# Performance work log

Hardware: AMD Instinct MI355X
Metric: run time of the kernel (lower is better)

Reference implementation:

```python
import jax, jax.numpy as jnp
import numpy as np

NUM_HEADS = 16
BN_EPS = 1e-3  # tf.layers.BatchNormalization default epsilon


def _z_norm(a, axis, scale):
    mu = jnp.mean(a, axis=axis, keepdims=True)
    sd = jnp.std(a, axis=axis, keepdims=True)
    return (a - mu) / (sd * scale + 1e-10)


def setup_inputs() -> dict:
    key = jax.random.key(0)
    ks = jax.random.split(key, 12)
    B, S, D = 4, 1024, 1024
    w = lambda k: jax.random.normal(k, (D, D), dtype=jnp.float32) * 0.02
    return {
        'q': jax.random.normal(ks[0], (B, S, D), dtype=jnp.float32),
        'k': jax.random.normal(ks[1], (B, S, D), dtype=jnp.float32),
        'v': jax.random.normal(ks[2], (B, S, D), dtype=jnp.float32),
        'mask': jax.random.randint(ks[3], (B, 1, S, S), 0, 2, dtype=jnp.int32),
        'is_training': 0,
        'q_gamma': jnp.ones((D,), jnp.float32),
        'q_beta': jnp.zeros((D,), jnp.float32),
        'q_mean': jax.random.normal(ks[4], (D,), dtype=jnp.float32) * 0.1,
        'q_var': jnp.ones((D,), jnp.float32),
        'Wq': w(ks[5]), 'bq': jnp.zeros((D,), jnp.float32),
        'Wqq': w(ks[6]), 'bqq': jnp.zeros((D,), jnp.float32),
        'Wo': w(ks[7]), 'bo': jnp.zeros((D,), jnp.float32),
    }


def reference(q, k, v, mask, is_training, q_gamma, q_beta, q_mean, q_var,
              Wq, bq, Wqq, bqq, Wo, bo):
    B, S, D = q.shape
    H = NUM_HEADS
    dh = D // H
    # BatchNorm (inference mode: call() passes no training flag -> moving stats)
    x = (q - q_mean) * jax.lax.rsqrt(q_var + BN_EPS) * q_gamma + q_beta
    # q = wqq(relu(wq(.)))  (k/v projections are dead: call() sets k = v = q)
    x = jax.nn.relu(x @ Wq + bq)
    x = x @ Wqq + bqq
    qh = x.reshape(B, S, H, dh).transpose(0, 2, 1, 3)  # [B,H,S,dh]
    logits = jnp.einsum('bhqd,bhkd->bhqk', qh, qh) / jnp.sqrt(jnp.float32(dh))
    logits = logits + mask.astype(logits.dtype) * -1e9
    attn = jax.nn.softmax(logits, axis=3)  # [B,H,S,S]
    last = jnp.mean(logits, axis=-1, keepdims=True)        # [B,H,S,1]
    last2 = jnp.mean(logits, axis=(2, 3), keepdims=True)   # [B,H,1,1]
    w_within = jax.nn.softmax(_z_norm(last, 2, 2), axis=2)   # softmax over queries
    w_betw = jax.nn.softmax(_z_norm(last2, 1, 2), axis=1)    # softmax over heads
    attn = attn * w_within * w_betw
    out = jnp.einsum('bhqk,bhkd->bhqd', attn, qh)           # v == qh
    out = out.transpose(0, 2, 1, 3).reshape(B, S, D)
    out = out @ Wo + bo
    return out, attn
```

## Files before the change

### kernel.cpp

```cpp
#include <hip/hip_runtime.h>
#include <math.h>


constexpr int Bz = 4, S = 1024, D = 1024, H = 16, DH = 64;
constexpr int N_ROWS = Bz * S;
#define BN_EPS 1e-3f
#define NEG_BIG -1e9f

typedef __attribute__((ext_vector_type(8))) short bf16x8;
typedef __attribute__((ext_vector_type(8))) unsigned short u16x8;
typedef __attribute__((ext_vector_type(4))) unsigned short u16x4;
typedef __attribute__((ext_vector_type(4))) float f32x4;

__device__ inline unsigned short f2bf(float f) {
  union { float f; unsigned int u; } v; v.f = f;
  unsigned int u = v.u;
  return (unsigned short)((u + 0x7FFFu + ((u >> 16) & 1u)) >> 16);
}
__device__ inline float bf2f(unsigned short h) {
  union { unsigned int u; float f; } v; v.u = ((unsigned int)h) << 16;
  return v.f;
}

__global__ __launch_bounds__(256)
void k_prep_all(const float* __restrict__ W0, const float* __restrict__ W1,
                const float* __restrict__ W2, unsigned short* __restrict__ T0,
                unsigned short* __restrict__ T1, unsigned short* __restrict__ T2,
                const float* __restrict__ q, const float* __restrict__ gamma,
                const float* __restrict__ beta, const float* __restrict__ mean,
                const float* __restrict__ var, unsigned short* __restrict__ qbn,
                const int* __restrict__ mask, float* __restrict__ n_cnt2,
                float* __restrict__ cs) {
  __shared__ float Ls[64][65];
  const int bid = blockIdx.x, t = threadIdx.x;
  if (bid < 768) {
    const int z = bid >> 8, rem = bid & 255;
    const float* W = z == 0 ? W0 : (z == 1 ? W1 : W2);
    unsigned short* T = z == 0 ? T0 : (z == 1 ? T1 : T2);
    const int k0 = (rem & 15) * 64, n0 = (rem >> 4) * 64;
    {
      const int r = t >> 2, c0 = (t & 3) * 16;
#pragma unroll
      for (int i = 0; i < 4; ++i) {
        float4 f = *(const float4*)&W[(size_t)(k0 + r) * 1024 + n0 + c0 + 4 * i];
        Ls[r][c0 + 4 * i] = f.x; Ls[r][c0 + 4 * i + 1] = f.y;
        Ls[r][c0 + 4 * i + 2] = f.z; Ls[r][c0 + 4 * i + 3] = f.w;
      }
    }
    __syncthreads();
    {
      const int d = t >> 2, c = t & 3;
      u16x8 o0, o1;
#pragma unroll
      for (int i = 0; i < 8; ++i) {
        o0[i] = f2bf(Ls[c * 16 + i][d]);
        o1[i] = f2bf(Ls[c * 16 + 8 + i][d]);
      }
      unsigned short* dst = &T[(size_t)(n0 + d) * 1024 + k0 + c * 16];
      *(u16x8*)dst = o0;
      *(u16x8*)(dst + 8) = o1;
    }
  } else if (bid < 2816) {
    const int id = bid - 768;
    const size_t e0 = ((size_t)id * 256 + t) * 8;
    const int col = (int)(e0 & 1023);
    float x[8], g[8], bb[8], mm[8], vv[8];
    *(float4*)&x[0] = *(const float4*)&q[e0];
    *(float4*)&x[4] = *(const float4*)&q[e0 + 4];
    *(float4*)&g[0] = *(const float4*)&gamma[col];
    *(float4*)&g[4] = *(const float4*)&gamma[col + 4];
    *(float4*)&bb[0] = *(const float4*)&beta[col];
    *(float4*)&bb[4] = *(const float4*)&beta[col + 4];
    *(float4*)&mm[0] = *(const float4*)&mean[col];
    *(float4*)&mm[4] = *(const float4*)&mean[col + 4];
    *(float4*)&vv[0] = *(const float4*)&var[col];
    *(float4*)&vv[4] = *(const float4*)&var[col + 4];
    bf16x8 o;
#pragma unroll
    for (int i = 0; i < 8; ++i) {
      float sc = g[i] * rsqrtf(vv[i] + BN_EPS);
      o[i] = (short)f2bf(fmaf(x[i], sc, bb[i] - mm[i] * sc));
    }
    *(bf16x8*)&qbn[e0] = o;
  } else if (bid < 2880) {
    const int id = bid - 2816;
    const int row = id * 64 + (t >> 2);
    const int4* mp = (const int4*)&mask[(size_t)row * 1024 + (t & 3) * 256];
    int s = 0;
#pragma unroll 8
    for (int i = 0; i < 64; ++i) { int4 m = mp[i]; s += (m.x + m.y) + (m.z + m.w); }
    s += __shfl_xor(s, 1, 64);
    s += __shfl_xor(s, 2, 64);
    if ((t & 3) == 0) n_cnt2[row] = (float)s;
  } else {
    const int id = bid - 2880;
    *(float4*)&cs[id * 1024 + t * 4] = make_float4(0.f, 0.f, 0.f, 0.f);
  }
}

template<bool RELU, bool OUTBF>
__global__ __launch_bounds__(256)
void k_gemm2(const unsigned short* __restrict__ A, const unsigned short* __restrict__ BT,
             const float* __restrict__ bias, void* __restrict__ C) {
  __shared__ unsigned short As[128 * 64];
  __shared__ unsigned short Bs[64 * 64];
  const int t = threadIdx.x;
  const int w = t >> 6, l = t & 63, l15 = l & 15, l4 = l >> 4;
  const int m0 = blockIdx.x * 128, n0 = blockIdx.y * 64;
  const int wm = (w >> 1) * 64, wn = (w & 1) * 32;

  f32x4 acc[4][2];
#pragma unroll
  for (int i = 0; i < 4; ++i)
#pragma unroll
    for (int j = 0; j < 2; ++j) acc[i][j] = (f32x4){0.f, 0.f, 0.f, 0.f};

  for (int k0 = 0; k0 < 1024; k0 += 64) {
    __syncthreads();
#pragma unroll
    for (int i = 0; i < 4; ++i) {
      const int c = i * 256 + t, row = c >> 3, slot = c & 7;
      bf16x8 v = *(const bf16x8*)&A[(size_t)(m0 + row) * 1024 + k0 + slot * 8];
      *(bf16x8*)((char*)As + row * 128 + ((slot * 16) ^ ((row & 7) << 4))) = v;
    }
#pragma unroll
    for (int i = 0; i < 2; ++i) {
      const int c = i * 256 + t, row = c >> 3, slot = c & 7;
      bf16x8 v = *(const bf16x8*)&BT[(size_t)(n0 + row) * 1024 + k0 + slot * 8];
      *(bf16x8*)((char*)Bs + row * 128 + ((slot * 16) ^ ((row & 7) << 4))) = v;
    }
    __syncthreads();
    bf16x8 af[4][2], bfr[2][2];
#pragma unroll
    for (int bm = 0; bm < 4; ++bm) {
      const int r = wm + bm * 16 + l15;
#pragma unroll
      for (int kk = 0; kk < 2; ++kk)
        af[bm][kk] = *(const bf16x8*)((const char*)As + r * 128 +
                                      ((kk * 64 + l4 * 16) ^ ((r & 7) << 4)));
    }
#pragma unroll
    for (int bn = 0; bn < 2; ++bn) {
      const int r = wn + bn * 16 + l15;
#pragma unroll
      for (int kk = 0; kk < 2; ++kk)
        bfr[bn][kk] = *(const bf16x8*)((const char*)Bs + r * 128 +
                                       ((kk * 64 + l4 * 16) ^ ((r & 7) << 4)));
    }
#pragma unroll
    for (int bm = 0; bm < 4; ++bm)
#pragma unroll
      for (int bn = 0; bn < 2; ++bn) {
        acc[bm][bn] = __builtin_amdgcn_mfma_f32_16x16x32_bf16(af[bm][0], bfr[bn][0], acc[bm][bn], 0, 0, 0);
        acc[bm][bn] = __builtin_amdgcn_mfma_f32_16x16x32_bf16(af[bm][1], bfr[bn][1], acc[bm][bn], 0, 0, 0);
      }
  }
  float bv[2];
#pragma unroll
  for (int bn = 0; bn < 2; ++bn) bv[bn] = bias[n0 + wn + bn * 16 + l15];
#pragma unroll
  for (int bm = 0; bm < 4; ++bm)
#pragma unroll
    for (int bn = 0; bn < 2; ++bn)
#pragma unroll
      for (int r = 0; r < 4; ++r) {
        float v = acc[bm][bn][r] + bv[bn];
        if (RELU) v = fmaxf(v, 0.f);
        const size_t idx = (size_t)(m0 + wm + bm * 16 + l4 * 4 + r) * 1024 +
                           n0 + wn + bn * 16 + l15;
        if (OUTBF) ((unsigned short*)C)[idx] = f2bf(v);
        else ((float*)C)[idx] = v;
      }
}

__global__ __launch_bounds__(256)
void k_cvt(const unsigned short* __restrict__ xqb, unsigned short* __restrict__ qhT,
           float* __restrict__ cs) {
  __shared__ unsigned short Ls[64][72];
  const int t = threadIdx.x;
  const int b = blockIdx.x >> 4;
  const int sb = (blockIdx.x & 15) * 64;
  const int h = blockIdx.y;
  {
    const int r = t >> 2, c0 = (t & 3) * 16;
    const unsigned short* src = &xqb[(size_t)(b * 1024 + sb + r) * 1024 + h * 64 + c0];
    u16x8 a = *(const u16x8*)src;
    u16x8 b8 = *(const u16x8*)(src + 8);
    *(u16x8*)&Ls[r][c0] = a;
    *(u16x8*)&Ls[r][c0 + 8] = b8;
  }
  __syncthreads();
  {
    const int d = t >> 2, c = t & 3;
    u16x8 o0, o1;
#pragma unroll
    for (int i = 0; i < 8; ++i) {
      o0[i] = Ls[c * 16 + i][d];
      o1[i] = Ls[c * 16 + 8 + i][d];
    }
    unsigned short* dst = &qhT[(size_t)((b * 16 + h) * 64 + d) * 1024 + sb + c * 16];
    *(u16x8*)dst = o0;
    *(u16x8*)(dst + 8) = o1;
  }
  if (t < 64) {
    float s = 0.f;
#pragma unroll 8
    for (int i = 0; i < 64; ++i) s += bf2f(Ls[i][t]);
    atomicAdd(&cs[b * 1024 + h * 64 + t], s);
  }
}

__global__ __launch_bounds__(256)
void k_suml2(const unsigned short* __restrict__ xqb, const float* __restrict__ cs,
             float* __restrict__ sum_l) {
  const int qc = blockIdx.x, b = blockIdx.y;
  const int t = threadIdx.x;
  const int h = t >> 4, dg = t & 15;
  const float4 c4 = *(const float4*)&cs[b * 1024 + t * 4];
  for (int qi = 0; qi < 64; ++qi) {
    const int q = qc * 64 + qi;
    u16x4 xv = *(const u16x4*)&xqb[(size_t)(b * 1024 + q) * 1024 + t * 4];
    float s = bf2f(xv[0]) * c4.x + bf2f(xv[1]) * c4.y +
              bf2f(xv[2]) * c4.z + bf2f(xv[3]) * c4.w;
    s += __shfl_xor(s, 1, 64);
    s += __shfl_xor(s, 2, 64);
    s += __shfl_xor(s, 4, 64);
    s += __shfl_xor(s, 8, 64);
    if (dg == 0) sum_l[(size_t)(b * 16 + h) * 1024 + q] = s * 0.125f;
  }
}

template<int PASS>
__global__ __launch_bounds__(256)
void k_attn5(const unsigned short* __restrict__ xqb, const int* __restrict__ mask,
             const unsigned short* __restrict__ qhT, const float* __restrict__ w_row,
             float* __restrict__ attn, unsigned short* __restrict__ pvb,
             float* __restrict__ denom) {
  __shared__ unsigned short Ks[2][64 * 64];
  __shared__ unsigned short Pst[PASS ? 4 * 16 * 64 : 8];

  const int t = threadIdx.x;
  const int w = t >> 6, l = t & 63;
  const int l15 = l & 15, l4 = l >> 4;
  const int q0 = blockIdx.x * 64;
  const int h = blockIdx.y, b = blockIdx.z;
  const int bh = b * 16 + h;

  bf16x8 qa0, qa1;
  {
    const unsigned short* qp =
        &xqb[(size_t)(b * 1024 + q0 + w * 16 + l15) * 1024 + h * 64 + l4 * 8];
    qa0 = *(const bf16x8*)qp;
    qa1 = *(const bf16x8*)(qp + 32);
  }

  float wsc[4];
  if (PASS == 1) {
#pragma unroll
    for (int r = 0; r < 4; ++r)
      wsc[r] = w_row[(size_t)bh * 1024 + q0 + w * 16 + l4 * 4 + r];
  }

  float dsum[4] = {0.f, 0.f, 0.f, 0.f};
  f32x4 vacc[4];
#pragma unroll
  for (int c = 0; c < 4; ++c) vacc[c] = (f32x4){0.f, 0.f, 0.f, 0.f};

  const int srow = t >> 3, sslot = t & 7;
  const int sswz = (sslot * 16) ^ ((srow & 7) << 4);
  const size_t sga = (size_t)(b * 1024 + srow) * 1024 + h * 64 + sslot * 8;

  bf16x8 s0 = *(const bf16x8*)&xqb[sga];
  bf16x8 s1 = *(const bf16x8*)&xqb[sga + 32 * 1024];
  *(bf16x8*)((char*)Ks[0] + srow * 128 + sswz) = s0;
  *(bf16x8*)((char*)Ks[0] + (srow + 32) * 128 + sswz) = s1;
  s0 = *(const bf16x8*)&xqb[sga + 64 * 1024];
  s1 = *(const bf16x8*)&xqb[sga + 96 * 1024];

  for (int ti = 0; ti < 16; ++ti) {
    __syncthreads();
    const int cur = ti & 1;
    if (ti < 15) {
      *(bf16x8*)((char*)Ks[cur ^ 1] + srow * 128 + sswz) = s0;
      *(bf16x8*)((char*)Ks[cur ^ 1] + (srow + 32) * 128 + sswz) = s1;
    }
    if (ti < 14) {
      s0 = *(const bf16x8*)&xqb[sga + (size_t)(ti + 2) * 65536];
      s1 = *(const bf16x8*)&xqb[sga + (size_t)(ti + 2) * 65536 + 32 * 1024];
    }
    const int k0 = ti * 64;

    f32x4 lacc[4];
#pragma unroll
    for (int c = 0; c < 4; ++c) {
      const int r = c * 16 + l15;
      const char* kb = (const char*)Ks[cur] + r * 128;
      const int rsw = (r & 7) << 4;
      bf16x8 kb0 = *(const bf16x8*)(kb + ((l4 * 16) ^ rsw));
      bf16x8 kb1 = *(const bf16x8*)(kb + ((64 + l4 * 16) ^ rsw));
      f32x4 z = (f32x4){0.f, 0.f, 0.f, 0.f};
      z = __builtin_amdgcn_mfma_f32_16x16x32_bf16(qa0, kb0, z, 0, 0, 0);
      z = __builtin_amdgcn_mfma_f32_16x16x32_bf16(qa1, kb1, z, 0, 0, 0);
      lacc[c] = z;
    }

    int mrr[4][4];
#pragma unroll
    for (int c = 0; c < 4; ++c)
#pragma unroll
      for (int r = 0; r < 4; ++r)
        mrr[c][r] = mask[(size_t)(b * 1024 + q0 + w * 16 + l4 * 4 + r) * 1024 +
                         k0 + c * 16 + l15];

#pragma unroll
    for (int c = 0; c < 4; ++c) {
#pragma unroll
      for (int r = 0; r < 4; ++r) {
        float p = __expf(fmaf((float)mrr[c][r], NEG_BIG, lacc[c][r] * 0.125f));
        if (PASS == 0) {
          dsum[r] += p;
        } else {
          attn[(size_t)(bh * 1024 + q0 + w * 16 + l4 * 4 + r) * 1024 +
               k0 + c * 16 + l15] = p * wsc[r];
          const int qq = l4 * 4 + r;
          *(unsigned short*)((char*)&Pst[w * 1024] + qq * 128 +
                             (((c * 16 + l15) * 2) ^ ((qq & 7) << 4))) = f2bf(p);
        }
      }
    }

    if (PASS == 1) {
#pragma unroll
      for (int kk = 0; kk < 2; ++kk) {
        const char* pb = (const char*)&Pst[w * 1024] + l15 * 128;
        bf16x8 pa = *(const bf16x8*)(pb + ((kk * 64 + l4 * 16) ^ ((l15 & 7) << 4)));
#pragma unroll
        for (int c = 0; c < 4; ++c) {
          bf16x8 vb = *(const bf16x8*)&qhT[(size_t)(bh * 64 + c * 16 + l15) * 1024 +
                                           k0 + kk * 32 + l4 * 8];
          vacc[c] = __builtin_amdgcn_mfma_f32_16x16x32_bf16(pa, vb, vacc[c], 0, 0, 0);
        }
      }
    }
  }

  if (PASS == 0) {
#pragma unroll
    for (int r = 0; r < 4; ++r) {
      float d2 = dsum[r];
#pragma unroll
      for (int m = 1; m < 16; m <<= 1) d2 += __shfl_xor(d2, m, 64);
      if (l15 == 0)
        denom[(size_t)bh * 1024 + q0 + w * 16 + l4 * 4 + r] = d2;
    }
  } else {
#pragma unroll
    for (int c = 0; c < 4; ++c)
#pragma unroll
      for (int r = 0; r < 4; ++r)
        pvb[(size_t)(b * 1024 + q0 + w * 16 + l4 * 4 + r) * 1024 +
            h * 64 + c * 16 + l15] = f2bf(vacc[c][r] * wsc[r]);
  }
}

__global__ __launch_bounds__(256)
void k_wwithin(const float* __restrict__ sum_l, const float* __restrict__ n_cnt2,
               const float* __restrict__ denom, float* __restrict__ w_row) {
  __shared__ double buf[1024];
  __shared__ double red[256];
  __shared__ double sh_mu, sh_sd, sh_zm, sh_es;
  const int bh = blockIdx.x, t = threadIdx.x;
  const int base = bh << 10;
  const int nbase = (bh >> 4) << 10;
  double part = 0;
  for (int q2 = t; q2 < 1024; q2 += 256) {
    double last = ((double)sum_l[base + q2] - 1e9 * (double)n_cnt2[nbase + q2]) * (1.0 / 1024.0);
    buf[q2] = last; part += last;
  }
  red[t] = part; __syncthreads();
  for (int s2 = 128; s2 > 0; s2 >>= 1) { if (t < s2) red[t] += red[t + s2]; __syncthreads(); }
  if (t == 0) sh_mu = red[0] * (1.0 / 1024.0);
  __syncthreads();
  const double mu = sh_mu;
  part = 0;
  for (int q2 = t; q2 < 1024; q2 += 256) { double d = buf[q2] - mu; part += d * d; }
  red[t] = part; __syncthreads();
  for (int s2 = 128; s2 > 0; s2 >>= 1) { if (t < s2) red[t] += red[t + s2]; __syncthreads(); }
  if (t == 0) sh_sd = sqrt(red[0] * (1.0 / 1024.0));
  __syncthreads();
  const double dn = sh_sd * 2.0 + 1e-10;
  part = -1e300;
  for (int q2 = t; q2 < 1024; q2 += 256) {
    double z = (buf[q2] - mu) / dn;
    buf[q2] = z;
    part = fmax(part, z);
  }
  red[t] = part; __syncthreads();
  for (int s2 = 128; s2 > 0; s2 >>= 1) { if (t < s2) red[t] = fmax(red[t], red[t + s2]); __syncthreads(); }
  if (t == 0) sh_zm = red[0];
  __syncthreads();
  const double zm = sh_zm;
  part = 0;
  for (int q2 = t; q2 < 1024; q2 += 256) {
    double e = exp(buf[q2] - zm);
    buf[q2] = e; part += e;
  }
  red[t] = part; __syncthreads();
  for (int s2 = 128; s2 > 0; s2 >>= 1) { if (t < s2) red[t] += red[t + s2]; __syncthreads(); }
  if (t == 0) sh_es = red[0];
  __syncthreads();
  const double tot = sh_es;
  for (int q2 = t; q2 < 1024; q2 += 256) {
    w_row[base + q2] = (float)(buf[q2] / tot * 0.0625 / (double)denom[base + q2]);
  }
}

extern "C" void kernel_launch(void* const* d_in, const int* in_sizes, int n_in,
                              void* d_out, int out_size, void* d_ws, size_t ws_size,
                              hipStream_t stream) {
  const float* q      = (const float*)d_in[0];
  const int*   mask   = (const int*)d_in[3];
  const float* q_gamma = (const float*)d_in[5];
  const float* q_beta  = (const float*)d_in[6];
  const float* q_mean  = (const float*)d_in[7];
  const float* q_var   = (const float*)d_in[8];
  const float* Wq  = (const float*)d_in[9];
  const float* bq  = (const float*)d_in[10];
  const float* Wqq = (const float*)d_in[11];
  const float* bqq = (const float*)d_in[12];
  const float* Wo  = (const float*)d_in[13];
  const float* bo  = (const float*)d_in[14];

  float* out  = (float*)d_out;
  float* attn = (float*)d_out + (size_t)N_ROWS * D;
  unsigned short* xqb = (unsigned short*)d_out;

  char* ws = (char*)d_ws;
  unsigned short* x1b = (unsigned short*)(ws);
  unsigned short* qhT = (unsigned short*)(ws + (8u << 20));
  unsigned short* pvb = (unsigned short*)(ws + (16u << 20));
  unsigned short* qbn = (unsigned short*)(ws + (24u << 20));
  unsigned short* WqT  = (unsigned short*)(ws + (32u << 20));
  unsigned short* WqqT = (unsigned short*)(ws + (34u << 20));
  unsigned short* WoT  = (unsigned short*)(ws + (36u << 20));
  float* cs     = (float*)(ws + (38u << 20));
  float* sum_l  = cs + 4096;
  float* denom  = sum_l + 65536;
  float* w_row  = denom + 65536;
  float* n_cnt2 = w_row + 65536;

  k_prep_all<<<2884, 256, 0, stream>>>(Wq, Wqq, Wo, WqT, WqqT, WoT,
                                       q, q_gamma, q_beta, q_mean, q_var, qbn,
                                       mask, n_cnt2, cs);

  dim3 gg(32, 16);
  k_gemm2<true, true><<<gg, 256, 0, stream>>>(qbn, WqT, bq, x1b);
  k_gemm2<false, true><<<gg, 256, 0, stream>>>(x1b, WqqT, bqq, xqb);

  k_cvt<<<dim3(64, 16), 256, 0, stream>>>(xqb, qhT, cs);
  k_suml2<<<dim3(16, 4), 256, 0, stream>>>(xqb, cs, sum_l);

  dim3 ga(16, 16, 4);
  k_attn5<0><<<ga, 256, 0, stream>>>(xqb, mask, nullptr, nullptr, nullptr, nullptr, denom);
  k_wwithin<<<Bz * H, 256, 0, stream>>>(sum_l, n_cnt2, denom, w_row);
  k_attn5<1><<<ga, 256, 0, stream>>>(xqb, mask, qhT, w_row, attn, pvb, nullptr);

  k_gemm2<false, false><<<gg, 256, 0, stream>>>(pvb, WoT, bo, out);
}
```

Before: 258.1 us.

## Fuse BatchNorm into first GEMM and column sums into second GEMM epilogue

The separate BatchNorm pass that wrote a bf16 copy of q is removed. The first GEMM now reads fp32 q directly and applies precomputed per-column scale and shift while staging A tiles. Column sums of the projected queries are accumulated with atomics in the second GEMM's epilogue rather than in k_cvt, and the per-row sum_l dot product moves into k_wwithin, which drops the k_suml2 kernel. This saves a full activation write and read plus one launch, at the cost of doubling A-tile global traffic in GEMM1 and putting more serial work into the 64-block k_wwithin.

```diff
diff --git a/kernel.cpp b/kernel.cpp
--- a/kernel.cpp
+++ b/kernel.cpp
@@ -9,7 +9,6 @@
 
 typedef __attribute__((ext_vector_type(8))) short bf16x8;
 typedef __attribute__((ext_vector_type(8))) unsigned short u16x8;
-typedef __attribute__((ext_vector_type(4))) unsigned short u16x4;
 typedef __attribute__((ext_vector_type(4))) float f32x4;
 
 __device__ inline unsigned short f2bf(float f) {
@@ -21,14 +20,26 @@
   union { unsigned int u; float f; } v; v.u = ((unsigned int)h) << 16;
   return v.f;
 }
+__device__ inline bf16x8 pack8(float4 a, float4 b) {
+  bf16x8 v;
+  v[0] = (short)f2bf(a.x); v[1] = (short)f2bf(a.y);
+  v[2] = (short)f2bf(a.z); v[3] = (short)f2bf(a.w);
+  v[4] = (short)f2bf(b.x); v[5] = (short)f2bf(b.y);
+  v[6] = (short)f2bf(b.z); v[7] = (short)f2bf(b.w);
+  return v;
+}
+__device__ inline float4 bnf(float4 f, float4 s, float4 sh) {
+  return make_float4(fmaf(f.x, s.x, sh.x), fmaf(f.y, s.y, sh.y),
+                     fmaf(f.z, s.z, sh.z), fmaf(f.w, s.w, sh.w));
+}
 
 __global__ __launch_bounds__(256)
 void k_prep_all(const float* __restrict__ W0, const float* __restrict__ W1,
                 const float* __restrict__ W2, unsigned short* __restrict__ T0,
                 unsigned short* __restrict__ T1, unsigned short* __restrict__ T2,
-                const float* __restrict__ q, const float* __restrict__ gamma,
-                const float* __restrict__ beta, const float* __restrict__ mean,
-                const float* __restrict__ var, unsigned short* __restrict__ qbn,
+                const float* __restrict__ gamma, const float* __restrict__ beta,
+                const float* __restrict__ mean, const float* __restrict__ var,
+                float* __restrict__ bnsc, float* __restrict__ bnsh,
                 const int* __restrict__ mask, float* __restrict__ n_cnt2,
                 float* __restrict__ cs) {
   __shared__ float Ls[64][65];
@@ -60,30 +71,8 @@
       *(u16x8*)dst = o0;
       *(u16x8*)(dst + 8) = o1;
     }
-  } else if (bid < 2816) {
+  } else if (bid < 832) {
     const int id = bid - 768;
-    const size_t e0 = ((size_t)id * 256 + t) * 8;
-    const int col = (int)(e0 & 1023);
-    float x[8], g[8], bb[8], mm[8], vv[8];
-    *(float4*)&x[0] = *(const float4*)&q[e0];
-    *(float4*)&x[4] = *(const float4*)&q[e0 + 4];
-    *(float4*)&g[0] = *(const float4*)&gamma[col];
-    *(float4*)&g[4] = *(const float4*)&gamma[col + 4];
-    *(float4*)&bb[0] = *(const float4*)&beta[col];
-    *(float4*)&bb[4] = *(const float4*)&beta[col + 4];
-    *(float4*)&mm[0] = *(const float4*)&mean[col];
-    *(float4*)&mm[4] = *(const float4*)&mean[col + 4];
-    *(float4*)&vv[0] = *(const float4*)&var[col];
-    *(float4*)&vv[4] = *(const float4*)&var[col + 4];
-    bf16x8 o;
-#pragma unroll
-    for (int i = 0; i < 8; ++i) {
-      float sc = g[i] * rsqrtf(vv[i] + BN_EPS);
-      o[i] = (short)f2bf(fmaf(x[i], sc, bb[i] - mm[i] * sc));
-    }
-    *(bf16x8*)&qbn[e0] = o;
-  } else if (bid < 2880) {
-    const int id = bid - 2816;
     const int row = id * 64 + (t >> 2);
     const int4* mp = (const int4*)&mask[(size_t)row * 1024 + (t & 3) * 256];
     int s = 0;
@@ -92,16 +81,23 @@
     s += __shfl_xor(s, 1, 64);
     s += __shfl_xor(s, 2, 64);
     if ((t & 3) == 0) n_cnt2[row] = (float)s;
+  } else if (bid < 836) {
+    const int id = bid - 832;
+    *(float4*)&cs[id * 1024 + t * 4] = make_float4(0.f, 0.f, 0.f, 0.f);
   } else {
-    const int id = bid - 2880;
-    *(float4*)&cs[id * 1024 + t * 4] = make_float4(0.f, 0.f, 0.f, 0.f);
-  }
-}
-
-template<bool RELU, bool OUTBF>
+    const int i = (bid - 836) * 256 + t;
+    float sc = gamma[i] * rsqrtf(var[i] + BN_EPS);
+    bnsc[i] = sc;
+    bnsh[i] = beta[i] - mean[i] * sc;
+  }
+}
+
+template<int AMODE, bool RELU, bool OUTBF, bool CSUM>
 __global__ __launch_bounds__(256)
-void k_gemm2(const unsigned short* __restrict__ A, const unsigned short* __restrict__ BT,
-             const float* __restrict__ bias, void* __restrict__ C) {
+void k_gemm2n(const void* __restrict__ Asrc, const unsigned short* __restrict__ BT,
+              const float* __restrict__ bias, void* __restrict__ C,
+              const float* __restrict__ bnsc, const float* __restrict__ bnsh,
+              float* __restrict__ cs) {
   __shared__ unsigned short As[128 * 64];
   __shared__ unsigned short Bs[64 * 64];
   const int t = threadIdx.x;
@@ -120,7 +116,18 @@
 #pragma unroll
     for (int i = 0; i < 4; ++i) {
       const int c = i * 256 + t, row = c >> 3, slot = c & 7;
-      bf16x8 v = *(const bf16x8*)&A[(size_t)(m0 + row) * 1024 + k0 + slot * 8];
+      bf16x8 v;
+      if (AMODE == 0) {
+        v = *(const bf16x8*)&((const unsigned short*)Asrc)[(size_t)(m0 + row) * 1024 + k0 + slot * 8];
+      } else {
+        const float* ap = &((const float*)Asrc)[(size_t)(m0 + row) * 1024 + k0 + slot * 8];
+        float4 f0 = *(const float4*)ap, f1 = *(const float4*)(ap + 4);
+        float4 s0 = *(const float4*)&bnsc[k0 + slot * 8];
+        float4 s1 = *(const float4*)&bnsc[k0 + slot * 8 + 4];
+        float4 h0 = *(const float4*)&bnsh[k0 + slot * 8];
+        float4 h1 = *(const float4*)&bnsh[k0 + slot * 8 + 4];
+        v = pack8(bnf(f0, s0, h0), bnf(f1, s1, h1));
+      }
       *(bf16x8*)((char*)As + row * 128 + ((slot * 16) ^ ((row & 7) << 4))) = v;
     }
 #pragma unroll
@@ -158,6 +165,7 @@
   float bv[2];
 #pragma unroll
   for (int bn = 0; bn < 2; ++bn) bv[bn] = bias[n0 + wn + bn * 16 + l15];
+  float csum[2] = {0.f, 0.f};
 #pragma unroll
   for (int bm = 0; bm < 4; ++bm)
 #pragma unroll
@@ -166,16 +174,26 @@
       for (int r = 0; r < 4; ++r) {
         float v = acc[bm][bn][r] + bv[bn];
         if (RELU) v = fmaxf(v, 0.f);
+        if (CSUM) csum[bn] += v;
         const size_t idx = (size_t)(m0 + wm + bm * 16 + l4 * 4 + r) * 1024 +
                            n0 + wn + bn * 16 + l15;
         if (OUTBF) ((unsigned short*)C)[idx] = f2bf(v);
         else ((float*)C)[idx] = v;
       }
+  if (CSUM) {
+#pragma unroll
+    for (int bn = 0; bn < 2; ++bn) {
+      float s = csum[bn];
+      s += __shfl_xor(s, 16, 64);
+      s += __shfl_xor(s, 32, 64);
+      if (l4 == 0)
+        atomicAdd(&cs[(m0 >> 10) * 1024 + n0 + wn + bn * 16 + l15], s);
+    }
+  }
 }
 
 __global__ __launch_bounds__(256)
-void k_cvt(const unsigned short* __restrict__ xqb, unsigned short* __restrict__ qhT,
-           float* __restrict__ cs) {
+void k_cvt(const unsigned short* __restrict__ xqb, unsigned short* __restrict__ qhT) {
   __shared__ unsigned short Ls[64][72];
   const int t = threadIdx.x;
   const int b = blockIdx.x >> 4;
@@ -202,32 +220,6 @@
     *(u16x8*)dst = o0;
     *(u16x8*)(dst + 8) = o1;
   }
-  if (t < 64) {
-    float s = 0.f;
-#pragma unroll 8
-    for (int i = 0; i < 64; ++i) s += bf2f(Ls[i][t]);
-    atomicAdd(&cs[b * 1024 + h * 64 + t], s);
-  }
-}
-
-__global__ __launch_bounds__(256)
-void k_suml2(const unsigned short* __restrict__ xqb, const float* __restrict__ cs,
-             float* __restrict__ sum_l) {
-  const int qc = blockIdx.x, b = blockIdx.y;
-  const int t = threadIdx.x;
-  const int h = t >> 4, dg = t & 15;
-  const float4 c4 = *(const float4*)&cs[b * 1024 + t * 4];
-  for (int qi = 0; qi < 64; ++qi) {
-    const int q = qc * 64 + qi;
-    u16x4 xv = *(const u16x4*)&xqb[(size_t)(b * 1024 + q) * 1024 + t * 4];
-    float s = bf2f(xv[0]) * c4.x + bf2f(xv[1]) * c4.y +
-              bf2f(xv[2]) * c4.z + bf2f(xv[3]) * c4.w;
-    s += __shfl_xor(s, 1, 64);
-    s += __shfl_xor(s, 2, 64);
-    s += __shfl_xor(s, 4, 64);
-    s += __shfl_xor(s, 8, 64);
-    if (dg == 0) sum_l[(size_t)(b * 16 + h) * 1024 + q] = s * 0.125f;
-  }
 }
 
 template<int PASS>
@@ -364,17 +356,33 @@
 }
 
 __global__ __launch_bounds__(256)
-void k_wwithin(const float* __restrict__ sum_l, const float* __restrict__ n_cnt2,
-               const float* __restrict__ denom, float* __restrict__ w_row) {
+void k_wwithin(const unsigned short* __restrict__ xqb, const float* __restrict__ cs,
+               const float* __restrict__ n_cnt2, const float* __restrict__ denom,
+               float* __restrict__ w_row) {
   __shared__ double buf[1024];
   __shared__ double red[256];
+  __shared__ float csl[64];
   __shared__ double sh_mu, sh_sd, sh_zm, sh_es;
   const int bh = blockIdx.x, t = threadIdx.x;
   const int base = bh << 10;
-  const int nbase = (bh >> 4) << 10;
+  const int b = bh >> 4, h = bh & 15;
+  const int nbase = b << 10;
+  if (t < 64) csl[t] = cs[b * 1024 + h * 64 + t];
+  __syncthreads();
   double part = 0;
-  for (int q2 = t; q2 < 1024; q2 += 256) {
-    double last = ((double)sum_l[base + q2] - 1e9 * (double)n_cnt2[nbase + q2]) * (1.0 / 1024.0);
+  for (int j = 0; j < 4; ++j) {
+    const int q2 = t + j * 256;
+    const unsigned short* xr = &xqb[(size_t)(b * 1024 + q2) * 1024 + h * 64];
+    float s = 0.f;
+#pragma unroll
+    for (int dd = 0; dd < 64; dd += 8) {
+      u16x8 xv = *(const u16x8*)&xr[dd];
+      s += bf2f(xv[0]) * csl[dd]     + bf2f(xv[1]) * csl[dd + 1] +
+           bf2f(xv[2]) * csl[dd + 2] + bf2f(xv[3]) * csl[dd + 3] +
+           bf2f(xv[4]) * csl[dd + 4] + bf2f(xv[5]) * csl[dd + 5] +
+           bf2f(xv[6]) * csl[dd + 6] + bf2f(xv[7]) * csl[dd + 7];
+    }
+    double last = ((double)(s * 0.125f) - 1e9 * (double)n_cnt2[nbase + q2]) * (1.0 / 1024.0);
     buf[q2] = last; part += last;
   }
   red[t] = part; __syncthreads();
@@ -439,31 +447,30 @@
   unsigned short* x1b = (unsigned short*)(ws);
   unsigned short* qhT = (unsigned short*)(ws + (8u << 20));
   unsigned short* pvb = (unsigned short*)(ws + (16u << 20));
-  unsigned short* qbn = (unsigned short*)(ws + (24u << 20));
   unsigned short* WqT  = (unsigned short*)(ws + (32u << 20));
   unsigned short* WqqT = (unsigned short*)(ws + (34u << 20));
   unsigned short* WoT  = (unsigned short*)(ws + (36u << 20));
   float* cs     = (float*)(ws + (38u << 20));
-  float* sum_l  = cs + 4096;
-  float* denom  = sum_l + 65536;
+  float* denom  = cs + 4096;
   float* w_row  = denom + 65536;
   float* n_cnt2 = w_row + 65536;
-
-  k_prep_all<<<2884, 256, 0, stream>>>(Wq, Wqq, Wo, WqT, WqqT, WoT,
-                                       q, q_gamma, q_beta, q_mean, q_var, qbn,
-                                       mask, n_cnt2, cs);
+  float* bnsc   = n_cnt2 + 4096;
+  float* bnsh   = bnsc + 1024;
+
+  k_prep_all<<<840, 256, 0, stream>>>(Wq, Wqq, Wo, WqT, WqqT, WoT,
+                                      q_gamma, q_beta, q_mean, q_var, bnsc, bnsh,
+                                      mask, n_cnt2, cs);
 
   dim3 gg(32, 16);
-  k_gemm2<true, true><<<gg, 256, 0, stream>>>(qbn, WqT, bq, x1b);
-  k_gemm2<false, true><<<gg, 256, 0, stream>>>(x1b, WqqT, bqq, xqb);
-
-  k_cvt<<<dim3(64, 16), 256, 0, stream>>>(xqb, qhT, cs);
-  k_suml2<<<dim3(16, 4), 256, 0, stream>>>(xqb, cs, sum_l);
+  k_gemm2n<1, true, true, false><<<gg, 256, 0, stream>>>(q, WqT, bq, x1b, bnsc, bnsh, nullptr);
+  k_gemm2n<0, false, true, true><<<gg, 256, 0, stream>>>(x1b, WqqT, bqq, xqb, nullptr, nullptr, cs);
+
+  k_cvt<<<dim3(64, 16), 256, 0, stream>>>(xqb, qhT);
 
   dim3 ga(16, 16, 4);
   k_attn5<0><<<ga, 256, 0, stream>>>(xqb, mask, nullptr, nullptr, nullptr, nullptr, denom);
-  k_wwithin<<<Bz * H, 256, 0, stream>>>(sum_l, n_cnt2, denom, w_row);
+  k_wwithin<<<Bz * H, 256, 0, stream>>>(xqb, cs, n_cnt2, denom, w_row);
   k_attn5<1><<<ga, 256, 0, stream>>>(xqb, mask, qhT, w_row, attn, pvb, nullptr);
 
-  k_gemm2<false, false><<<gg, 256, 0, stream>>>(pvb, WoT, bo, out);
-}
+  k_gemm2n<0, false, false, false><<<gg, 256, 0, stream>>>(pvb, WoT, bo, out, nullptr, nullptr, nullptr);
+}
```

Result: faster. 247.4 us (-4.1%).
